# Kernel tuning notes

Measured on AMD Instinct MI355X. Metric: run time of the kernel, lower is better.

Reference implementation:

```python
import jax, jax.numpy as jnp
import numpy as np

B, T, D = 2, 2048, 2048
N_HEADS, N_KV = 16, 4
HD = D // N_HEADS  # 128
ROPE_BASE = 10000.0


def _rope_tables(t, dim, base=ROPE_BASE):
    inv_freq = 1.0 / (base ** (jnp.arange(0, dim, 2, dtype=jnp.float32) / dim))
    freqs = jnp.arange(t, dtype=jnp.float32)[:, None] * inv_freq[None, :]  # (T, dim/2)
    emb = jnp.concatenate([freqs, freqs], axis=-1)  # (T, dim)
    return jnp.cos(emb), jnp.sin(emb)


def _rotate_half(x):
    x1, x2 = jnp.split(x, 2, axis=-1)
    return jnp.concatenate([-x2, x1], axis=-1)


def _apply_rope(x, cos, sin):
    # x: (B, H, T, hd); cos/sin: (T, hd)
    return x * cos[None, None] + _rotate_half(x) * sin[None, None]


def setup_inputs() -> dict:
    key = jax.random.key(0)
    ks = jax.random.split(key, 5)
    s = 0.02
    return {
        "x": jax.random.normal(ks[0], (B, T, D), jnp.float32),
        "wq": jax.random.normal(ks[1], (D, N_HEADS * HD), jnp.float32) * s,
        "wk": jax.random.normal(ks[2], (D, N_KV * HD), jnp.float32) * s,
        "wv": jax.random.normal(ks[3], (D, N_KV * HD), jnp.float32) * s,
        "wo": jax.random.normal(ks[4], (D, D), jnp.float32) * s,
    }


def reference(x, wq, wk, wv, wo):
    b, t, c = x.shape
    n_rep = N_HEADS // N_KV
    scale = 1.0 / np.sqrt(HD)

    q = (x @ wq).reshape(b, t, N_HEADS, HD).transpose(0, 2, 1, 3)  # (B,H,T,hd)
    k = (x @ wk).reshape(b, t, N_KV, HD).transpose(0, 2, 1, 3)     # (B,Hkv,T,hd)
    v = (x @ wv).reshape(b, t, N_KV, HD).transpose(0, 2, 1, 3)

    cos, sin = _rope_tables(t, HD)
    q = _apply_rope(q, cos, sin)
    k = _apply_rope(k, cos, sin)

    # repeat_kv (GQA)
    k = jnp.repeat(k, n_rep, axis=1)  # (B,H,T,hd)
    v = jnp.repeat(v, n_rep, axis=1)

    scores = jnp.einsum("bhqd,bhkd->bhqk", q, k) * scale
    causal = jnp.tril(jnp.ones((t, t), dtype=bool))
    scores = jnp.where(causal[None, None], scores, -jnp.inf)
    attn = jax.nn.softmax(scores, axis=-1)
    out = jnp.einsum("bhqk,bhkd->bhqd", attn, v)
    out = out.transpose(0, 2, 1, 3).reshape(b, t, c)
    return out @ wo
```

## Files before the change

### kernel.cpp

```cpp
#include <hip/hip_runtime.h>
#include <hip/hip_bf16.h>
#include <math.h>

#define B_   2
#define T_   2048
#define D_   2048
#define NH_  16
#define NKV_ 4
#define HD_  128
#define MROWS (B_*T_)
#define NQKV  (NH_*HD_ + 2*NKV_*HD_)

typedef __bf16 bf16_t;
typedef __bf16 bf16x8 __attribute__((ext_vector_type(8)));
typedef float  floatx4 __attribute__((ext_vector_type(4)));

__device__ __forceinline__ void async_copy16(const bf16_t* gsrc, bf16_t* ldst) {
  __builtin_amdgcn_global_load_lds(
      (const __attribute__((address_space(1))) unsigned int*)gsrc,
      (__attribute__((address_space(3))) unsigned int*)ldst, 16, 0, 0);
}

__global__ void cast_f32_bf16(const float* __restrict__ src, bf16_t* __restrict__ dst, int n) {
  int i = (blockIdx.x * 256 + threadIdx.x) * 8;
  if (i >= n) return;
  float4 a = *(const float4*)(src + i);
  float4 b = *(const float4*)(src + i + 4);
  bf16x8 v;
  v[0]=(bf16_t)a.x; v[1]=(bf16_t)a.y; v[2]=(bf16_t)a.z; v[3]=(bf16_t)a.w;
  v[4]=(bf16_t)b.x; v[5]=(bf16_t)b.y; v[6]=(bf16_t)b.z; v[7]=(bf16_t)b.w;
  *(bf16x8*)(dst + i) = v;
}

__global__ void transpose_cast(const float* __restrict__ src, bf16_t* __restrict__ dst,
                               int K, int N) {
  __shared__ float tile[32][33];
  int n0 = blockIdx.x * 32, k0 = blockIdx.y * 32;
  int tx = threadIdx.x, ty = threadIdx.y;
#pragma unroll
  for (int r = 0; r < 4; r++)
    tile[ty + r*8][tx] = src[(size_t)(k0 + ty + r*8) * N + n0 + tx];
  __syncthreads();
#pragma unroll
  for (int r = 0; r < 4; r++)
    dst[(size_t)(n0 + ty + r*8) * K + k0 + tx] = (bf16_t)tile[tx][ty + r*8];
}

template <typename OUT_T>
__global__ __launch_bounds__(256, 2)
void gemm_bt(const bf16_t* __restrict__ A, const bf16_t* __restrict__ Bt,
             OUT_T* __restrict__ C, int M, int N, int K) {
  __shared__ __align__(16) bf16_t As[128 * 64];
  __shared__ __align__(16) bf16_t Bs[128 * 64];
  const int tid  = threadIdx.x;
  const int wave = tid >> 6, lane = tid & 63;
  const int quad = lane >> 4, l16 = lane & 15;
  const int nBlocksM = M >> 7;
  const int bm = blockIdx.x % nBlocksM, bn = blockIdx.x / nBlocksM;
  const int m0 = bm * 128, n0 = bn * 128;
  const int wm = (wave >> 1) * 64, wn = (wave & 1) * 64;

  floatx4 acc[4][4];
#pragma unroll
  for (int i = 0; i < 4; i++)
#pragma unroll
    for (int j = 0; j < 4; j++) acc[i][j] = floatx4{0.f, 0.f, 0.f, 0.f};

  for (int k0 = 0; k0 < K; k0 += 64) {
    __syncthreads();
#pragma unroll
    for (int i = 0; i < 4; i++) {
      int e = i * 256 + tid;
      int row = e >> 3, grp = e & 7;
      int gg = grp ^ (row & 7);
      async_copy16(A + (size_t)(m0 + row) * K + k0 + gg * 8, As + e * 8);
    }
#pragma unroll
    for (int i = 0; i < 4; i++) {
      int e = i * 256 + tid;
      int row = e >> 3, grp = e & 7;
      int gg = grp ^ (row & 7);
      async_copy16(Bt + (size_t)(n0 + row) * K + k0 + gg * 8, Bs + e * 8);
    }
    __syncthreads();
#pragma unroll
    for (int ks = 0; ks < 2; ks++) {
      bf16x8 af[4], bfr[4];
      int grp = ks * 4 + quad;
#pragma unroll
      for (int mi = 0; mi < 4; mi++) {
        int row = wm + mi * 16 + l16;
        af[mi] = *(const bf16x8*)(As + row * 64 + ((grp ^ (row & 7)) << 3));
      }
#pragma unroll
      for (int ni = 0; ni < 4; ni++) {
        int row = wn + ni * 16 + l16;
        bfr[ni] = *(const bf16x8*)(Bs + row * 64 + ((grp ^ (row & 7)) << 3));
      }
#pragma unroll
      for (int mi = 0; mi < 4; mi++)
#pragma unroll
        for (int ni = 0; ni < 4; ni++)
          acc[mi][ni] = __builtin_amdgcn_mfma_f32_16x16x32_bf16(af[mi], bfr[ni], acc[mi][ni], 0, 0, 0);
    }
  }
#pragma unroll
  for (int mi = 0; mi < 4; mi++) {
#pragma unroll
    for (int r = 0; r < 4; r++) {
      int row = m0 + wm + mi * 16 + quad * 4 + r;
      size_t base = (size_t)row * N + n0 + wn;
#pragma unroll
      for (int ni = 0; ni < 4; ni++)
        C[base + ni * 16 + l16] = (OUT_T)acc[mi][ni][r];
    }
  }
}

__global__ void rope_scatter(const bf16_t* __restrict__ qkv,
                             bf16_t* __restrict__ Qb, bf16_t* __restrict__ Kb) {
  int g = blockIdx.x * 256 + threadIdx.x;
  int j = g & 63;
  int rest = g >> 6;
  int head = rest % (NH_ + NKV_);
  int row  = rest / (NH_ + NKV_);
  int t = row & (T_ - 1);
  int b = row >> 11;
  const bf16_t* src = qkv + (size_t)row * NQKV;
  float ang = (float)t * expf(-0.14391156816f * (float)j);
  float sn, cs;
  sincosf(ang, &sn, &cs);
  if (head < NH_) {
    float x0 = (float)src[head * HD_ + j];
    float x1 = (float)src[head * HD_ + 64 + j];
    const float scale = 0.12751651541057752f;
    bf16_t* dst = Qb + ((size_t)(b * NH_ + head) * T_ + t) * HD_;
    dst[j]      = (bf16_t)((x0 * cs - x1 * sn) * scale);
    dst[j + 64] = (bf16_t)((x1 * cs + x0 * sn) * scale);
  } else {
    int kvh = head - NH_;
    float x0 = (float)src[NH_ * HD_ + kvh * HD_ + j];
    float x1 = (float)src[NH_ * HD_ + kvh * HD_ + 64 + j];
    bf16_t* dst = Kb + ((size_t)(b * NKV_ + kvh) * T_ + t) * HD_;
    dst[j]      = (bf16_t)(x0 * cs - x1 * sn);
    dst[j + 64] = (bf16_t)(x1 * cs + x0 * sn);
  }
}

__global__ void v_transpose(const bf16_t* __restrict__ qkv, bf16_t* __restrict__ Vt) {
  __shared__ float tile[32][33];
  int t0 = blockIdx.x * 32, d0 = blockIdx.y * 32;
  int bk = blockIdx.z;
  int b = bk / NKV_, kvh = bk % NKV_;
  int tx = threadIdx.x, ty = threadIdx.y;
#pragma unroll
  for (int r = 0; r < 4; r++) {
    int t = t0 + ty + r * 8;
    tile[ty + r*8][tx] =
        (float)qkv[(size_t)(b * T_ + t) * NQKV + (NH_ + NKV_) * HD_ + kvh * HD_ + d0 + tx];
  }
  __syncthreads();
#pragma unroll
  for (int r = 0; r < 4; r++) {
    int d = d0 + ty + r * 8;
    Vt[((size_t)(b * NKV_ + kvh) * HD_ + d) * T_ + t0 + tx] = (bf16_t)tile[tx][ty + r*8];
  }
}

__global__ __launch_bounds__(256, 2)
void flash_attn(const bf16_t* __restrict__ Qb, const bf16_t* __restrict__ Kb,
                const bf16_t* __restrict__ Vt, bf16_t* __restrict__ Ob) {
  __shared__ __align__(16) bf16_t Ks[2][64 * 128];
  __shared__ __align__(16) bf16_t Vs[2][128 * 64];
  __shared__ __align__(16) bf16_t Ps[4][16 * 72];

  const int tid = threadIdx.x;
  const int wave = tid >> 6, lane = tid & 63;
  const int quad = lane >> 4, l16 = lane & 15;
  const int nQT = T_ / 64;
  const int bid = blockIdx.x;
  const int bh = bid % (B_ * NH_);
  const int qt = (nQT - 1) - (bid / (B_ * NH_));
  const int h = bh % NH_;
  const int b = bh / NH_;
  const int kv = h >> 2;

  const bf16_t* qbase = Qb + ((size_t)(b * NH_ + h) * T_ + qt * 64) * HD_;
  const bf16_t* kbase = Kb + ((size_t)(b * NKV_ + kv) * T_) * HD_;
  const bf16_t* vbase = Vt + ((size_t)(b * NKV_ + kv) * HD_) * T_;

  auto stage = [&](int kt, int bufi) {
#pragma unroll
    for (int i = 0; i < 4; i++) {
      int e = i * 256 + tid;
      int row = e >> 4, grp = e & 15;
      int gg = grp ^ (row & 15);
      async_copy16(kbase + (size_t)(kt * 64 + row) * HD_ + gg * 8, &Ks[bufi][e * 8]);
    }
#pragma unroll
    for (int i = 0; i < 4; i++) {
      int e = i * 256 + tid;
      int row = e >> 3, grp = e & 7;
      int gg = grp ^ (row & 7);
      async_copy16(vbase + (size_t)row * T_ + kt * 64 + gg * 8, &Vs[bufi][e * 8]);
    }
  };

  stage(0, 0);

  bf16x8 qf[4];
  {
    const bf16_t* qptr = qbase + (wave * 16 + l16) * HD_;
#pragma unroll
    for (int ks = 0; ks < 4; ks++)
      qf[ks] = *(const bf16x8*)(qptr + ks * 32 + quad * 8);
  }

  floatx4 o[8];
#pragma unroll
  for (int i = 0; i < 8; i++) o[i] = floatx4{0.f, 0.f, 0.f, 0.f};
  float m_r[4], l_r[4];
#pragma unroll
  for (int r = 0; r < 4; r++) { m_r[r] = -1e30f; l_r[r] = 0.f; }

  for (int kt = 0; kt <= qt; kt++) {
    const int bufi = kt & 1;
    __syncthreads();
    if (kt < qt) stage(kt + 1, bufi ^ 1);

    floatx4 s[4];
#pragma unroll
    for (int nt = 0; nt < 4; nt++) s[nt] = floatx4{0.f, 0.f, 0.f, 0.f};
#pragma unroll
    for (int ks = 0; ks < 4; ks++) {
      int grp = ks * 4 + quad;
#pragma unroll
      for (int nt = 0; nt < 4; nt++) {
        int row = nt * 16 + l16;
        bf16x8 kf = *(const bf16x8*)(&Ks[bufi][row * 128 + ((grp ^ (row & 15)) << 3)]);
        s[nt] = __builtin_amdgcn_mfma_f32_16x16x32_bf16(qf[ks], kf, s[nt], 0, 0, 0);
      }
    }

    if (kt == qt) {
#pragma unroll
      for (int nt = 0; nt < 4; nt++)
#pragma unroll
        for (int r = 0; r < 4; r++) {
          int kg = nt * 16 + l16;
          int qg = wave * 16 + quad * 4 + r;
          if (kg > qg) s[nt][r] = -1e30f;
        }
    }

#pragma unroll
    for (int r = 0; r < 4; r++) {
      float mx = fmaxf(fmaxf(s[0][r], s[1][r]), fmaxf(s[2][r], s[3][r]));
#pragma unroll
      for (int off = 1; off < 16; off <<= 1)
        mx = fmaxf(mx, __shfl_xor(mx, off, 64));
      float mnew = fmaxf(m_r[r], mx);
      float alpha = __builtin_amdgcn_exp2f(m_r[r] - mnew);
      m_r[r] = mnew;
      float sum = 0.f;
#pragma unroll
      for (int nt = 0; nt < 4; nt++) {
        float p = __builtin_amdgcn_exp2f(s[nt][r] - mnew);
        s[nt][r] = p;
        sum += p;
      }
#pragma unroll
      for (int off = 1; off < 16; off <<= 1)
        sum += __shfl_xor(sum, off, 64);
      l_r[r] = l_r[r] * alpha + sum;
#pragma unroll
      for (int nto = 0; nto < 8; nto++) o[nto][r] *= alpha;
    }

#pragma unroll
    for (int nt = 0; nt < 4; nt++)
#pragma unroll
      for (int r = 0; r < 4; r++)
        Ps[wave][(quad * 4 + r) * 72 + nt * 16 + l16] = (bf16_t)s[nt][r];

#pragma unroll
    for (int ks = 0; ks < 2; ks++) {
      bf16x8 pf = *(const bf16x8*)(&Ps[wave][l16 * 72 + ks * 32 + quad * 8]);
      int grp = ks * 4 + quad;
#pragma unroll
      for (int nt = 0; nt < 8; nt++) {
        int row = nt * 16 + l16;
        bf16x8 vf = *(const bf16x8*)(&Vs[bufi][row * 64 + ((grp ^ (row & 7)) << 3)]);
        o[nt] = __builtin_amdgcn_mfma_f32_16x16x32_bf16(pf, vf, o[nt], 0, 0, 0);
      }
    }
  }

#pragma unroll
  for (int r = 0; r < 4; r++) {
    int qg = qt * 64 + wave * 16 + quad * 4 + r;
    float inv_l = 1.f / l_r[r];
    size_t base = ((size_t)(b * T_) + qg) * D_ + h * HD_;
#pragma unroll
    for (int nt = 0; nt < 8; nt++)
      Ob[base + nt * 16 + l16] = (bf16_t)(o[nt][r] * inv_l);
  }
}

extern "C" void kernel_launch(void* const* d_in, const int* in_sizes, int n_in,
                              void* d_out, int out_size, void* d_ws, size_t ws_size,
                              hipStream_t stream) {
  const float* x  = (const float*)d_in[0];
  const float* wq = (const float*)d_in[1];
  const float* wk = (const float*)d_in[2];
  const float* wv = (const float*)d_in[3];
  const float* wo = (const float*)d_in[4];
  float* out = (float*)d_out;

  bf16_t* x_bf   = (bf16_t*)d_ws;
  bf16_t* attn_o = x_bf;
  bf16_t* wqkv_t = x_bf + (size_t)MROWS * D_;
  bf16_t* wo_t   = wqkv_t + (size_t)NQKV * D_;
  bf16_t* qkv    = wo_t + (size_t)D_ * D_;
  bf16_t* Qb     = qkv + (size_t)MROWS * NQKV;
  bf16_t* Kb     = Qb + (size_t)B_ * NH_ * T_ * HD_;
  bf16_t* Vt     = Kb + (size_t)B_ * NKV_ * T_ * HD_;

  cast_f32_bf16<<<(MROWS * D_) / (256 * 8), 256, 0, stream>>>(x, x_bf, MROWS * D_);
  transpose_cast<<<dim3(64, 64), dim3(32, 8), 0, stream>>>(wq, wqkv_t, D_, 2048);
  transpose_cast<<<dim3(16, 64), dim3(32, 8), 0, stream>>>(wk, wqkv_t + (size_t)2048 * D_, D_, 512);
  transpose_cast<<<dim3(16, 64), dim3(32, 8), 0, stream>>>(wv, wqkv_t + (size_t)2560 * D_, D_, 512);
  transpose_cast<<<dim3(64, 64), dim3(32, 8), 0, stream>>>(wo, wo_t, D_, 2048);

  gemm_bt<bf16_t><<<(MROWS / 128) * (NQKV / 128), 256, 0, stream>>>(
      x_bf, wqkv_t, qkv, MROWS, NQKV, D_);

  rope_scatter<<<(MROWS * (NH_ + NKV_) * 64) / 256, 256, 0, stream>>>(qkv, Qb, Kb);
  v_transpose<<<dim3(T_ / 32, HD_ / 32, B_ * NKV_), dim3(32, 8), 0, stream>>>(qkv, Vt);

  flash_attn<<<B_ * NH_ * (T_ / 64), 256, 0, stream>>>(Qb, Kb, Vt, attn_o);

  gemm_bt<float><<<(MROWS / 128) * (D_ / 128), 256, 0, stream>>>(
      attn_o, wo_t, out, MROWS, D_, D_);
}
```

Before: 311.7 us.

## Transpose MFMA operands so each lane owns one query row in attention

Swaps the A/B operands of the QK^T and PV MFMAs so the accumulator layout puts one query row per lane and four keys (or head dims) in the register vector. Softmax max and sum reductions then need only two cross-lane shuffles instead of four per row across four rows. Running max and sum become per-lane scalars, and the P tile and output are written with 4-wide vector stores instead of scalar bf16 stores. The causal mask indices are rewritten to match the new layout.

```diff
diff --git a/kernel.cpp b/kernel.cpp
--- a/kernel.cpp
+++ b/kernel.cpp
@@ -13,6 +13,7 @@
 
 typedef __bf16 bf16_t;
 typedef __bf16 bf16x8 __attribute__((ext_vector_type(8)));
+typedef __bf16 bf16x4 __attribute__((ext_vector_type(4)));
 typedef float  floatx4 __attribute__((ext_vector_type(4)));
 
 __device__ __forceinline__ void async_copy16(const bf16_t* gsrc, bf16_t* ldst) {
@@ -219,9 +220,7 @@
   floatx4 o[8];
 #pragma unroll
   for (int i = 0; i < 8; i++) o[i] = floatx4{0.f, 0.f, 0.f, 0.f};
-  float m_r[4], l_r[4];
-#pragma unroll
-  for (int r = 0; r < 4; r++) { m_r[r] = -1e30f; l_r[r] = 0.f; }
+  float m_s = -1e30f, l_s = 0.f;
 
   for (int kt = 0; kt <= qt; kt++) {
     const int bufi = kt & 1;
@@ -238,72 +237,77 @@
       for (int nt = 0; nt < 4; nt++) {
         int row = nt * 16 + l16;
         bf16x8 kf = *(const bf16x8*)(&Ks[bufi][row * 128 + ((grp ^ (row & 15)) << 3)]);
-        s[nt] = __builtin_amdgcn_mfma_f32_16x16x32_bf16(qf[ks], kf, s[nt], 0, 0, 0);
+        s[nt] = __builtin_amdgcn_mfma_f32_16x16x32_bf16(kf, qf[ks], s[nt], 0, 0, 0);
       }
     }
 
     if (kt == qt) {
+      int qlocal = wave * 16 + l16;
 #pragma unroll
       for (int nt = 0; nt < 4; nt++)
 #pragma unroll
         for (int r = 0; r < 4; r++) {
-          int kg = nt * 16 + l16;
-          int qg = wave * 16 + quad * 4 + r;
-          if (kg > qg) s[nt][r] = -1e30f;
+          int klocal = nt * 16 + quad * 4 + r;
+          if (klocal > qlocal) s[nt][r] = -1e30f;
         }
     }
 
-#pragma unroll
-    for (int r = 0; r < 4; r++) {
-      float mx = fmaxf(fmaxf(s[0][r], s[1][r]), fmaxf(s[2][r], s[3][r]));
-#pragma unroll
-      for (int off = 1; off < 16; off <<= 1)
-        mx = fmaxf(mx, __shfl_xor(mx, off, 64));
-      float mnew = fmaxf(m_r[r], mx);
-      float alpha = __builtin_amdgcn_exp2f(m_r[r] - mnew);
-      m_r[r] = mnew;
-      float sum = 0.f;
-#pragma unroll
-      for (int nt = 0; nt < 4; nt++) {
+    float mx = fmaxf(fmaxf(s[0][0], s[0][1]), fmaxf(s[0][2], s[0][3]));
+#pragma unroll
+    for (int nt = 1; nt < 4; nt++)
+      mx = fmaxf(mx, fmaxf(fmaxf(s[nt][0], s[nt][1]), fmaxf(s[nt][2], s[nt][3])));
+    mx = fmaxf(mx, __shfl_xor(mx, 16, 64));
+    mx = fmaxf(mx, __shfl_xor(mx, 32, 64));
+    float mnew = fmaxf(m_s, mx);
+    float alpha = __builtin_amdgcn_exp2f(m_s - mnew);
+    m_s = mnew;
+    float sum = 0.f;
+#pragma unroll
+    for (int nt = 0; nt < 4; nt++)
+#pragma unroll
+      for (int r = 0; r < 4; r++) {
         float p = __builtin_amdgcn_exp2f(s[nt][r] - mnew);
         s[nt][r] = p;
         sum += p;
       }
-#pragma unroll
-      for (int off = 1; off < 16; off <<= 1)
-        sum += __shfl_xor(sum, off, 64);
-      l_r[r] = l_r[r] * alpha + sum;
-#pragma unroll
-      for (int nto = 0; nto < 8; nto++) o[nto][r] *= alpha;
-    }
-
-#pragma unroll
-    for (int nt = 0; nt < 4; nt++)
-#pragma unroll
-      for (int r = 0; r < 4; r++)
-        Ps[wave][(quad * 4 + r) * 72 + nt * 16 + l16] = (bf16_t)s[nt][r];
+    sum += __shfl_xor(sum, 16, 64);
+    sum += __shfl_xor(sum, 32, 64);
+    l_s = l_s * alpha + sum;
+#pragma unroll
+    for (int dt = 0; dt < 8; dt++) o[dt] *= alpha;
+
+#pragma unroll
+    for (int nt = 0; nt < 4; nt++) {
+      bf16x4 p4;
+#pragma unroll
+      for (int r = 0; r < 4; r++) p4[r] = (bf16_t)s[nt][r];
+      *(bf16x4*)(&Ps[wave][l16 * 72 + nt * 16 + quad * 4]) = p4;
+    }
 
 #pragma unroll
     for (int ks = 0; ks < 2; ks++) {
       bf16x8 pf = *(const bf16x8*)(&Ps[wave][l16 * 72 + ks * 32 + quad * 8]);
       int grp = ks * 4 + quad;
 #pragma unroll
-      for (int nt = 0; nt < 8; nt++) {
-        int row = nt * 16 + l16;
+      for (int dt = 0; dt < 8; dt++) {
+        int row = dt * 16 + l16;
         bf16x8 vf = *(const bf16x8*)(&Vs[bufi][row * 64 + ((grp ^ (row & 7)) << 3)]);
-        o[nt] = __builtin_amdgcn_mfma_f32_16x16x32_bf16(pf, vf, o[nt], 0, 0, 0);
-      }
-    }
-  }
-
-#pragma unroll
-  for (int r = 0; r < 4; r++) {
-    int qg = qt * 64 + wave * 16 + quad * 4 + r;
-    float inv_l = 1.f / l_r[r];
+        o[dt] = __builtin_amdgcn_mfma_f32_16x16x32_bf16(vf, pf, o[dt], 0, 0, 0);
+      }
+    }
+  }
+
+  {
+    int qg = qt * 64 + wave * 16 + l16;
+    float inv_l = 1.f / l_s;
     size_t base = ((size_t)(b * T_) + qg) * D_ + h * HD_;
 #pragma unroll
-    for (int nt = 0; nt < 8; nt++)
-      Ob[base + nt * 16 + l16] = (bf16_t)(o[nt][r] * inv_l);
+    for (int dt = 0; dt < 8; dt++) {
+      bf16x4 w;
+#pragma unroll
+      for (int r = 0; r < 4; r++) w[r] = (bf16_t)(o[dt][r] * inv_l);
+      *(bf16x4*)(Ob + base + dt * 16 + quad * 4) = w;
+    }
   }
 }
 
```

Measured after the change: 280.5 us. -10.0%, faster.
